# Performance work log

Hardware: AMD Instinct MI355X
Metric: run time of the kernel (lower is better)

## Reference

```python
import jax, jax.numpy as jnp
import numpy as np

SESSION_CHANNELS = [128, 160, 192, 224, 240, 248, 252, 256]  # per-session channel counts
N_SESS = len(SESSION_CHANNELS)
B, MAX_C, MAX_T = 16, 256, 4096
HID, N_SRC = 512, 256


def setup_inputs() -> dict:
    key = jax.random.key(0)
    ks = jax.random.split(key, 7)
    session_ids = jax.random.randint(ks[0], (B,), 0, N_SESS)
    chan_table = jnp.asarray(SESSION_CHANNELS)
    channel_counts = chan_table[session_ids]
    seq_lens = jax.random.randint(ks[1], (B,), MAX_T // 2, MAX_T + 1)
    x = jax.random.normal(ks[2], (B, MAX_C, MAX_T), jnp.float32)
    # zero-pad beyond true channels and true time (as the docstring states)
    cmask = (jnp.arange(MAX_C)[None, :] < channel_counts[:, None]).astype(x.dtype)
    tmask = (jnp.arange(MAX_T)[None, :] < seq_lens[:, None]).astype(x.dtype)
    x = x * cmask[:, :, None] * tmask[:, None, :]
    # per-session Linear(num_channels -> HID), padded to MAX_C rows (torch-style uniform init)
    lim1 = 1.0 / np.sqrt(MAX_C)
    W_sess = jax.random.uniform(ks[3], (N_SESS, MAX_C, HID), jnp.float32, -lim1, lim1)
    b_sess = jax.random.uniform(ks[4], (N_SESS, HID), jnp.float32, -lim1, lim1)
    lim2 = 1.0 / np.sqrt(HID)
    W2 = jax.random.uniform(ks[5], (HID, N_SRC), jnp.float32, -lim2, lim2)
    b2 = jax.random.uniform(ks[6], (N_SRC,), jnp.float32, -lim2, lim2)
    return dict(x=x, session_ids=session_ids, channel_counts=channel_counts,
                seq_lens=seq_lens, W_sess=W_sess, b_sess=b_sess, W2=W2, b2=b2)


def reference(x, session_ids, channel_counts, seq_lens, W_sess, b_sess, W2, b2):
    # mask padded channels so the full-width contraction equals the sliced per-sample matmul
    cmask = (jnp.arange(x.shape[1])[None, :] < channel_counts[:, None]).astype(x.dtype)
    xm = x * cmask[:, :, None]                       # (B, Max_C, Max_T)
    W = W_sess[session_ids]                          # (B, Max_C, HID) gathered per sample
    b = b_sess[session_ids]                          # (B, HID)
    h = jnp.einsum('bct,bch->bht', xm, W) + b[:, :, None]
    h = jax.nn.gelu(h, approximate=False)            # torch nn.GELU default is exact erf
    out = jnp.einsum('bht,hs->bst', h, W2) + b2[None, :, None]  # (B, N_SRC, Max_T)
    tmask = (jnp.arange(x.shape[2])[None, :] < seq_lens[:, None]).astype(x.dtype)
    return out * tmask[:, None, :]
```

## Files before the change

### kernel.cpp

```cpp
#include <hip/hip_runtime.h>

typedef __attribute__((ext_vector_type(8))) _Float16 f16x8;
typedef __attribute__((ext_vector_type(4))) _Float16 f16x4;
typedef __attribute__((ext_vector_type(2))) __fp16 fp16v2;
typedef __attribute__((ext_vector_type(4))) float f32x4;

#define NB 16
#define MAXC 256
#define MAXT 4096
#define HID 512
#define NSRC 256

#define BARV() asm volatile("s_waitcnt vmcnt(0) lgkmcnt(0)\n\ts_barrier" ::: "memory")
#define BAR() asm volatile("s_waitcnt lgkmcnt(0)\n\ts_barrier" ::: "memory")

#define MFMA(a, b, c) __builtin_amdgcn_mfma_f32_16x16x32_f16(a, b, c, 0, 0, 0)

typedef __attribute__((address_space(1))) const void gconst_void;
typedef __attribute__((address_space(3))) void lds_void;
#define GLOAD16(gp, lp) \
  __builtin_amdgcn_global_load_lds((gconst_void*)(gp), (lds_void*)(lp), 16, 0, 0)

__device__ __forceinline__ float gelu_fast(float x) {
  float p = x * x;
  float q = __builtin_fmaf(p, -0.10294336f, -2.30220778f);
  float e = __builtin_amdgcn_exp2f(x * q);
  return x * __builtin_amdgcn_rcpf(1.0f + e);
}

__global__ void transpose_cvt_kernel(const float* __restrict__ src,
                                     _Float16* __restrict__ dst, int R, int C) {
  __shared__ float tile[32][33];
  const float* s = src + (size_t)blockIdx.z * R * C;
  _Float16* d = dst + (size_t)blockIdx.z * R * C;
  int c0 = blockIdx.x * 32, r0 = blockIdx.y * 32;
  int tx = threadIdx.x, ty = threadIdx.y;
  for (int i = ty; i < 32; i += 8)
    tile[i][tx] = s[(size_t)(r0 + i) * C + (c0 + tx)];
  __syncthreads();
  for (int i = ty; i < 32; i += 8)
    d[(size_t)(c0 + i) * R + (r0 + tx)] = (_Float16)tile[tx][i];
}

__global__ __launch_bounds__(256)
void transpose_x_kernel(const float* __restrict__ x,
                        const int* __restrict__ seq_lens,
                        const int* __restrict__ chan_counts,
                        _Float16* __restrict__ xT) {
  int b = blockIdx.z;
  int seqlen = seq_lens[b];
  int t0 = blockIdx.x * 64;
  if (t0 >= ((seqlen + 127) & ~127)) return;
  int c0 = blockIdx.y * 64;
  int tid = threadIdx.x;
  int wt = tid >> 5;
  int c2 = (tid & 31) * 2;
  _Float16* op = xT + ((size_t)b * MAXT + t0) * MAXC + c0;

  if (c0 >= chan_counts[b]) {
    #pragma unroll
    for (int i = 0; i < 8; ++i) {
      fp16v2 z = {(_Float16)0.f, (_Float16)0.f};
      *(fp16v2*)(op + (size_t)(wt + i * 8) * MAXC + c2) = z;
    }
    return;
  }

  __shared__ float tile[64][65];
  int tx = tid & 63, ty = tid >> 6;
  const float* xp = x + ((size_t)b * MAXC + c0) * MAXT + t0;
  #pragma unroll
  for (int i = 0; i < 16; ++i) {
    int c = ty + i * 4;
    tile[c][tx] = xp[(size_t)c * MAXT + tx];
  }
  __syncthreads();
  #pragma unroll
  for (int i = 0; i < 8; ++i) {
    int tl = wt + i * 8;
    fp16v2 p = __builtin_amdgcn_cvt_pkrtz(tile[c2][tl], tile[c2 + 1][tl]);
    *(fp16v2*)(op + (size_t)tl * MAXC + c2) = p;
  }
}


__global__ __launch_bounds__(256, 3)
void gemm1_kernel(const _Float16* __restrict__ xT,
                  const int* __restrict__ sess_ids,
                  const int* __restrict__ seq_lens,
                  const _Float16* __restrict__ W1t,
                  const float* __restrict__ b_sess,
                  _Float16* __restrict__ h_t) {
  int wg = blockIdx.x;
  int nt = wg & 63;
  int b = wg >> 6;
  int t0 = nt * 64;
  int seqlen = seq_lens[b];
  if (t0 >= seqlen) return;
  int sid = sess_ids[b];

  __shared__ _Float16 Bs[64 * 256];
  __shared__ _Float16 As[128 * 64];

  int tid = threadIdx.x;
  int lane = tid & 63, w = tid >> 6;
  int wr = w >> 1, wc = w & 1;
  int lg = lane >> 4, lr = lane & 15;

  {
    int l5 = lane >> 5, sl = lane & 31;
    const char* gB = (const char*)(xT + ((size_t)b * MAXT + t0) * MAXC);
    char* lB = (char*)Bs;
    #pragma unroll
    for (int j = 0; j < 8; ++j) {
      int g = w * 8 + j;
      int t = g * 2 + l5;
      int gc = (sl & 24) | ((sl & 7) ^ (t & 7));
      GLOAD16(gB + (size_t)t * 512 + gc * 16, lB + g * 1024);
    }
  }

  int rsub = lane >> 3;
  int swb = ((lane & 7) ^ rsub) * 16;
  const char* gA = (const char*)(W1t + (size_t)sid * HID * MAXC)
                   + (size_t)(w * 32 + rsub) * 512 + swb;
  char* lA = (char*)As + w * 4096;

#define STAGE_A(p)                                                            \
  {                                                                           \
    int nh0 = (p) >> 2, nkc = (p) & 3;                                        \
    _Pragma("unroll")                                                         \
    for (int j = 0; j < 4; ++j)                                               \
      GLOAD16(gA + (size_t)nh0 * 65536 + nkc * 128 + (size_t)j * 4096,        \
              lA + j * 1024);                                                 \
  }

  STAGE_A(0);

  f32x4 acc[4][2];
  #pragma unroll
  for (int mi = 0; mi < 4; ++mi) {
    f32x4 bv = *(const f32x4*)(b_sess + sid * HID + wr * 64 + mi * 16 + lg * 4);
    #pragma unroll
    for (int ni = 0; ni < 2; ++ni) acc[mi][ni] = bv;
  }

  BARV();

  _Float16* hp = h_t + (size_t)b * MAXT * HID;

  #pragma unroll 1
  for (int p = 0; p < 16; ++p) {
    int kc = p & 3;
    #pragma unroll
    for (int slot = 0; slot < 2; ++slot) {
      f16x8 af[4], bf[2];
      #pragma unroll
      for (int mi = 0; mi < 4; ++mi) {
        int row = wr * 64 + mi * 16 + lr;
        af[mi] = *(const f16x8*)(&As[row * 64 + (((slot * 4 + lg) ^ (row & 7)) * 8)]);
      }
      #pragma unroll
      for (int ni = 0; ni < 2; ++ni) {
        int t = wc * 32 + ni * 16 + lr;
        bf[ni] = *(const f16x8*)(&Bs[t * 256 + kc * 64 + (((slot * 4 + lg) ^ (t & 7)) * 8)]);
      }
      __builtin_amdgcn_s_setprio(1);
      #pragma unroll
      for (int mi = 0; mi < 4; ++mi)
        #pragma unroll
        for (int ni = 0; ni < 2; ++ni)
          acc[mi][ni] = MFMA(af[mi], bf[ni], acc[mi][ni]);
      __builtin_amdgcn_s_setprio(0);
    }
    if (p < 15) {
      BAR();
      STAGE_A(p + 1);
    }
    if (kc == 3) {
      int h0 = p >> 2;
      #pragma unroll
      for (int mi = 0; mi < 4; ++mi) {
        int h = h0 * 128 + wr * 64 + mi * 16 + lg * 4;
        #pragma unroll
        for (int ni = 0; ni < 2; ++ni) {
          int t = t0 + wc * 32 + ni * 16 + lr;
          f16x4 g;
          #pragma unroll
          for (int r = 0; r < 4; ++r) g[r] = (_Float16)gelu_fast(acc[mi][ni][r]);
          *(f16x4*)(hp + (size_t)t * HID + h) = g;
        }
      }
      if (p < 15) {
        #pragma unroll
        for (int mi = 0; mi < 4; ++mi) {
          f32x4 bv = *(const f32x4*)(b_sess + sid * HID + (h0 + 1) * 128 + wr * 64 + mi * 16 + lg * 4);
          #pragma unroll
          for (int ni = 0; ni < 2; ++ni) acc[mi][ni] = bv;
        }
      }
    }
    if (p < 15) BARV();
  }
}

__global__ __launch_bounds__(256, 4)
void gemm2_kernel(const int* __restrict__ seq_lens,
                  const _Float16* __restrict__ W2t,
                  const float* __restrict__ b2,
                  const _Float16* __restrict__ h_t,
                  float* __restrict__ out) {
  int wg = blockIdx.x;
  int nt = wg & 31;
  int mt = (wg >> 5) & 1;
  int b = wg >> 6;
  int tb0 = nt * 128, s0 = mt * 128;
  int seqlen = seq_lens[b];
  int tid = threadIdx.x;

  if (tb0 >= seqlen) {
    int sr = tid >> 1, tq = (tid & 1) * 64;
    float* po = out + ((size_t)b * NSRC + s0 + sr) * MAXT + tb0 + tq;
    f32x4 z = {0.f, 0.f, 0.f, 0.f};
    #pragma unroll
    for (int i = 0; i < 16; ++i) *(f32x4*)(po + i * 4) = z;
    return;
  }

  __shared__ _Float16 As[128 * 64];
  __shared__ _Float16 Bs[128 * 64];

  int lane = tid & 63, w = tid >> 6;
  int wr = w >> 1, wc = w & 1;
  int lg = lane >> 4, lr = lane & 15;

  f32x4 acc[4][4];
  #pragma unroll
  for (int mi = 0; mi < 4; ++mi) {
    f32x4 bv = *(const f32x4*)(b2 + s0 + wr * 64 + mi * 16 + lg * 4);
    #pragma unroll
    for (int ni = 0; ni < 4; ++ni) acc[mi][ni] = bv;
  }

  int rsub = lane >> 3;
  int swb = ((lane & 7) ^ rsub) * 16;
  const char* gA = (const char*)(W2t + (size_t)s0 * HID)
                   + (size_t)(w * 32 + rsub) * 1024 + swb;
  const char* gB = (const char*)(h_t + ((size_t)b * MAXT + tb0) * HID)
                   + (size_t)(w * 32 + rsub) * 1024 + swb;
  char* lA = (char*)As + w * 4096;
  char* lB = (char*)Bs + w * 4096;

#define STAGE2(kc)                                                    \
  _Pragma("unroll")                                                   \
  for (int j = 0; j < 4; ++j) {                                       \
    GLOAD16(gA + (size_t)(kc)*128 + (size_t)j * 8 * 1024, lA + j * 1024); \
    GLOAD16(gB + (size_t)(kc)*128 + (size_t)j * 8 * 1024, lB + j * 1024); \
  }

  STAGE2(0);
  BARV();

  #pragma unroll 1
  for (int kc = 0; kc < 8; ++kc) {
    #pragma unroll
    for (int slot = 0; slot < 2; ++slot) {
      f16x8 af[4], bf[4];
      #pragma unroll
      for (int mi = 0; mi < 4; ++mi) {
        int row = wr * 64 + mi * 16 + lr;
        af[mi] = *(const f16x8*)(&As[row * 64 + (((slot * 4 + lg) ^ (row & 7)) * 8)]);
      }
      #pragma unroll
      for (int ni = 0; ni < 4; ++ni) {
        int t = wc * 64 + ni * 16 + lr;
        bf[ni] = *(const f16x8*)(&Bs[t * 64 + (((slot * 4 + lg) ^ (t & 7)) * 8)]);
      }
      __builtin_amdgcn_s_setprio(1);
      #pragma unroll
      for (int mi = 0; mi < 4; ++mi)
        #pragma unroll
        for (int ni = 0; ni < 4; ++ni)
          acc[mi][ni] = MFMA(af[mi], bf[ni], acc[mi][ni]);
      __builtin_amdgcn_s_setprio(0);
    }
    if (kc < 7) {
      BAR();
      STAGE2(kc + 1);
      BARV();
    }
  }

  #pragma unroll
  for (int mi = 0; mi < 4; ++mi) {
    int s = s0 + wr * 64 + mi * 16 + lg * 4;
    #pragma unroll
    for (int ni = 0; ni < 4; ++ni) {
      int t = tb0 + wc * 64 + ni * 16 + lr;
      float m = (t < seqlen) ? 1.0f : 0.0f;
      #pragma unroll
      for (int r = 0; r < 4; ++r)
        out[((size_t)b * NSRC + s + r) * MAXT + t] = acc[mi][ni][r] * m;
    }
  }
}

extern "C" void kernel_launch(void* const* d_in, const int* in_sizes, int n_in,
                              void* d_out, int out_size, void* d_ws, size_t ws_size,
                              hipStream_t stream) {
  const float* x      = (const float*)d_in[0];
  const int* sess     = (const int*)d_in[1];
  const int* ccnt     = (const int*)d_in[2];
  const int* seq      = (const int*)d_in[3];
  const float* W_sess = (const float*)d_in[4];
  const float* b_sess = (const float*)d_in[5];
  const float* W2     = (const float*)d_in[6];
  const float* b2     = (const float*)d_in[7];
  float* out = (float*)d_out;

  char* wp = (char*)d_ws;
  _Float16* W1t = (_Float16*)wp;                     wp += (size_t)8 * HID * MAXC * 2;
  _Float16* W2t = (_Float16*)wp;                     wp += (size_t)NSRC * HID * 2;
  _Float16* h_t = (_Float16*)wp;                     wp += (size_t)NB * MAXT * HID * 2;
  _Float16* xT  = (_Float16*)wp;

  dim3 tb(32, 8);
  transpose_cvt_kernel<<<dim3(HID / 32, MAXC / 32, 8), tb, 0, stream>>>(W_sess, W1t, MAXC, HID);
  transpose_cvt_kernel<<<dim3(NSRC / 32, HID / 32, 1), tb, 0, stream>>>(W2, W2t, HID, NSRC);
  transpose_x_kernel<<<dim3(MAXT / 64, MAXC / 64, NB), dim3(256), 0, stream>>>(x, seq, ccnt, xT);

  gemm1_kernel<<<dim3(NB * 64), dim3(256), 0, stream>>>(xT, sess, seq, W1t, b_sess, h_t);
  gemm2_kernel<<<dim3(NB * 2 * 32), dim3(256), 0, stream>>>(seq, W2t, b2, h_t, out);
}
```

Baseline: 93.83 us.

## Double-buffer W1 tiles in gemm1 to overlap loads with MFMA

```diff
diff --git a/kernel.cpp b/kernel.cpp
--- a/kernel.cpp
+++ b/kernel.cpp
@@ -84,7 +84,7 @@
 }
 
 
-__global__ __launch_bounds__(256, 3)
+__global__ __launch_bounds__(256, 2)
 void gemm1_kernel(const _Float16* __restrict__ xT,
                   const int* __restrict__ sess_ids,
                   const int* __restrict__ seq_lens,
@@ -100,7 +100,7 @@
   int sid = sess_ids[b];
 
   __shared__ _Float16 Bs[64 * 256];
-  __shared__ _Float16 As[128 * 64];
+  __shared__ _Float16 As[2][128 * 64];
 
   int tid = threadIdx.x;
   int lane = tid & 63, w = tid >> 6;
@@ -110,13 +110,12 @@
   {
     int l5 = lane >> 5, sl = lane & 31;
     const char* gB = (const char*)(xT + ((size_t)b * MAXT + t0) * MAXC);
-    char* lB = (char*)Bs;
     #pragma unroll
     for (int j = 0; j < 8; ++j) {
       int g = w * 8 + j;
       int t = g * 2 + l5;
       int gc = (sl & 24) | ((sl & 7) ^ (t & 7));
-      GLOAD16(gB + (size_t)t * 512 + gc * 16, lB + g * 1024);
+      GLOAD16(gB + (size_t)t * 512 + gc * 16, (char*)Bs + g * 1024 + 0);
     }
   }
 
@@ -124,18 +123,14 @@
   int swb = ((lane & 7) ^ rsub) * 16;
   const char* gA = (const char*)(W1t + (size_t)sid * HID * MAXC)
                    + (size_t)(w * 32 + rsub) * 512 + swb;
-  char* lA = (char*)As + w * 4096;
-
-#define STAGE_A(p)                                                            \
-  {                                                                           \
-    int nh0 = (p) >> 2, nkc = (p) & 3;                                        \
-    _Pragma("unroll")                                                         \
-    for (int j = 0; j < 4; ++j)                                               \
-      GLOAD16(gA + (size_t)nh0 * 65536 + nkc * 128 + (size_t)j * 4096,        \
-              lA + j * 1024);                                                 \
-  }
-
-  STAGE_A(0);
+
+#define STAGE_A(p, bb)                                                        \
+  _Pragma("unroll")                                                           \
+  for (int j = 0; j < 4; ++j)                                                 \
+    GLOAD16(gA + (size_t)((p) >> 2) * 65536 + ((p)&3) * 128 + (size_t)j * 4096, \
+            (char*)As[bb] + w * 4096 + j * 1024);
+
+  STAGE_A(0, 0);
 
   f32x4 acc[4][2];
   #pragma unroll
@@ -151,14 +146,17 @@
 
   #pragma unroll 1
   for (int p = 0; p < 16; ++p) {
+    int cur = p & 1;
     int kc = p & 3;
+    if (p < 15) STAGE_A(p + 1, cur ^ 1);
+
     #pragma unroll
     for (int slot = 0; slot < 2; ++slot) {
       f16x8 af[4], bf[2];
       #pragma unroll
       for (int mi = 0; mi < 4; ++mi) {
         int row = wr * 64 + mi * 16 + lr;
-        af[mi] = *(const f16x8*)(&As[row * 64 + (((slot * 4 + lg) ^ (row & 7)) * 8)]);
+        af[mi] = *(const f16x8*)(&As[cur][row * 64 + (((slot * 4 + lg) ^ (row & 7)) * 8)]);
       }
       #pragma unroll
       for (int ni = 0; ni < 2; ++ni) {
@@ -173,15 +171,12 @@
           acc[mi][ni] = MFMA(af[mi], bf[ni], acc[mi][ni]);
       __builtin_amdgcn_s_setprio(0);
     }
-    if (p < 15) {
-      BAR();
-      STAGE_A(p + 1);
-    }
+
     if (kc == 3) {
-      int h0 = p >> 2;
+      int mt = p >> 2;
       #pragma unroll
       for (int mi = 0; mi < 4; ++mi) {
-        int h = h0 * 128 + wr * 64 + mi * 16 + lg * 4;
+        int h = mt * 128 + wr * 64 + mi * 16 + lg * 4;
         #pragma unroll
         for (int ni = 0; ni < 2; ++ni) {
           int t = t0 + wc * 32 + ni * 16 + lr;
@@ -194,7 +189,7 @@
       if (p < 15) {
         #pragma unroll
         for (int mi = 0; mi < 4; ++mi) {
-          f32x4 bv = *(const f32x4*)(b_sess + sid * HID + (h0 + 1) * 128 + wr * 64 + mi * 16 + lg * 4);
+          f32x4 bv = *(const f32x4*)(b_sess + sid * HID + (mt + 1) * 128 + wr * 64 + mi * 16 + lg * 4);
           #pragma unroll
           for (int ni = 0; ni < 2; ++ni) acc[mi][ni] = bv;
         }
```

Result: no change. 94.12 us (+0.3%).
